# Optimization experiments

Measured on AMD Instinct MI355X. Metric: run time of the kernel, lower is better.

## Reference

```python
import jax, jax.numpy as jnp
import numpy as np

EMBED_DIM = 1024
N_HEADS = 16
HEAD_DIM = EMBED_DIM // N_HEADS
B, T = 1, 4096

def setup_inputs() -> dict:
    key = jax.random.key(0)
    k1, k2, k3 = jax.random.split(key, 3)
    x = jax.random.normal(k1, (B, T, EMBED_DIM), dtype=jnp.float32)
    # match nn.Linear init scale roughly (not required for correctness testing)
    w_qkv = jax.random.normal(k2, (EMBED_DIM, 3 * EMBED_DIM), dtype=jnp.float32) * (EMBED_DIM ** -0.5)
    w_out = jax.random.normal(k3, (EMBED_DIM, EMBED_DIM), dtype=jnp.float32) * (EMBED_DIM ** -0.5)
    return {"x": x, "w_qkv": w_qkv, "w_out": w_out}

def reference(x, w_qkv, w_out):
    b, t, c = x.shape
    qkv = x @ w_qkv                                  # [B,T,3C]
    q, k, v = jnp.split(qkv, 3, axis=-1)
    # [B,T,C] -> [B,H,T,D]
    def heads(a):
        return a.reshape(b, t, N_HEADS, HEAD_DIM).transpose(0, 2, 1, 3)
    q, k, v = heads(q), heads(k), heads(v)
    scale = 1.0 / jnp.sqrt(jnp.asarray(HEAD_DIM, dtype=x.dtype))
    att = jnp.einsum('bhqd,bhkd->bhqk', q, k) * scale  # [B,H,T,T] (full matrix, as in source)
    att = jax.nn.softmax(att, axis=-1)
    y = jnp.einsum('bhqk,bhkd->bhqd', att, v)          # [B,H,T,D]
    y = y.transpose(0, 2, 1, 3).reshape(b, t, c)
    return y @ w_out
```

## Files before the change

kernel.cpp:

```cpp
#include <hip/hip_runtime.h>
#include <hip/hip_bf16.h>

#define T_SEQ 4096
#define C_DIM 1024
#define NH    16
#define HD    64
#define C3    3072

typedef __attribute__((ext_vector_type(8))) short short8;
typedef __attribute__((ext_vector_type(4))) short short4v;
typedef __attribute__((ext_vector_type(4))) float f32x4;
typedef __attribute__((ext_vector_type(16))) float f32x16;

__device__ __forceinline__ short f2bf(float f) {
  union { float f; unsigned u; } v; v.f = f;
  unsigned r = v.u + 0x7FFFu + ((v.u >> 16) & 1u);
  return (short)(r >> 16);
}

__device__ __forceinline__ unsigned cvt_pk_bf16(float lo, float hi) {
  unsigned r;
  asm volatile("v_cvt_pk_bf16_f32 %0, %1, %2" : "=v"(r) : "v"(lo), "v"(hi));
  return r;
}

__device__ __forceinline__ float exp2_fast(float x) {
  return __builtin_amdgcn_exp2f(x);
}

__device__ __forceinline__ float max_half64(float v) {
  return fmaxf(v, __shfl_xor(v, 32, 64));
}

__device__ __forceinline__ float m3(float a, float b, float c) {
  return fmaxf(fmaxf(a, b), c);
}

__device__ __forceinline__ void gld_lds16(const void* g, void* l) {
  __builtin_amdgcn_global_load_lds(
      (const __attribute__((address_space(1))) unsigned int*)g,
      (__attribute__((address_space(3))) unsigned int*)l, 16, 0, 0);
}

__global__ __launch_bounds__(256) void conv_bf16_kernel(const float* __restrict__ in,
                                                        short* __restrict__ out) {
  const size_t i = ((size_t)blockIdx.x * 256 + threadIdx.x) * 8;
  float4 v0 = *(const float4*)(in + i);
  float4 v1 = *(const float4*)(in + i + 4);
  short8 o;
  o[0] = f2bf(v0.x); o[1] = f2bf(v0.y); o[2] = f2bf(v0.z); o[3] = f2bf(v0.w);
  o[4] = f2bf(v1.x); o[5] = f2bf(v1.y); o[6] = f2bf(v1.z); o[7] = f2bf(v1.w);
  *(short8*)(out + i) = o;
}

__global__ void trans_conv_kernel(const float* __restrict__ in, short* __restrict__ out,
                                  int K, int N) {
  __shared__ float t[32][33];
  const int n0 = blockIdx.x * 32, k0 = blockIdx.y * 32;
  const int tx = threadIdx.x, ty = threadIdx.y;
  for (int i = ty; i < 32; i += 8) t[i][tx] = in[(size_t)(k0 + i) * N + n0 + tx];
  __syncthreads();
  for (int i = ty; i < 32; i += 8) out[(size_t)(n0 + i) * K + k0 + tx] = f2bf(t[tx][i]);
}

__device__ __forceinline__ void store_out(short* C, size_t idx, float v) { C[idx] = f2bf(v); }
__device__ __forceinline__ void store_out(float* C, size_t idx, float v) { C[idx] = v; }

template <typename OutT>
__global__ __launch_bounds__(256) void gemm_bt_kernel(const short* __restrict__ A,
                                                      const short* __restrict__ BT,
                                                      OutT* __restrict__ C,
                                                      int M, int N, int K) {
  __shared__ __align__(16) short As[128 * 32];
  __shared__ __align__(16) short Bs[128 * 32];
  const int tid = threadIdx.x;
  const int wid = tid >> 6;
  const int lane = tid & 63;
  const int l15 = lane & 15;
  const int l4 = lane >> 4;
  const int wr = wid >> 1;
  const int wc = wid & 1;
  const int bm = blockIdx.y * 128;
  const int bn = blockIdx.x * 128;

  f32x4 acc[4][4];
#pragma unroll
  for (int m = 0; m < 4; ++m)
#pragma unroll
    for (int n = 0; n < 4; ++n) acc[m][n] = (f32x4){0.f, 0.f, 0.f, 0.f};

  const int ebase = wid * 1024;
  const int e0 = ebase + lane * 8;
  const int r0 = e0 >> 5, c0 = e0 & 31;
  const int r1 = r0 + 16;

  for (int k0 = 0; k0 < K; k0 += 32) {
    __syncthreads();
    gld_lds16(A + (size_t)(bm + r0) * K + k0 + c0, As + ebase);
    gld_lds16(A + (size_t)(bm + r1) * K + k0 + c0, As + ebase + 512);
    gld_lds16(BT + (size_t)(bn + r0) * K + k0 + c0, Bs + ebase);
    gld_lds16(BT + (size_t)(bn + r1) * K + k0 + c0, Bs + ebase + 512);
    __syncthreads();

    short8 a[4], b[4];
#pragma unroll
    for (int m = 0; m < 4; ++m)
      a[m] = *(const short8*)&As[(wr * 64 + m * 16 + l15) * 32 + l4 * 8];
#pragma unroll
    for (int n = 0; n < 4; ++n)
      b[n] = *(const short8*)&Bs[(wc * 64 + n * 16 + l15) * 32 + l4 * 8];
#pragma unroll
    for (int m = 0; m < 4; ++m)
#pragma unroll
      for (int n = 0; n < 4; ++n)
        acc[m][n] = __builtin_amdgcn_mfma_f32_16x16x32_bf16(a[m], b[n], acc[m][n], 0, 0, 0);
  }

#pragma unroll
  for (int m = 0; m < 4; ++m) {
    const int row0 = bm + wr * 64 + m * 16 + l4 * 4;
#pragma unroll
    for (int n = 0; n < 4; ++n) {
      const int col = bn + wc * 64 + n * 16 + l15;
#pragma unroll
      for (int r = 0; r < 4; ++r)
        store_out(C, (size_t)(row0 + r) * N + col, acc[m][n][r]);
    }
  }
}

__global__ __launch_bounds__(256) void repack_v_kernel(const short* __restrict__ qkv,
                                                       short* __restrict__ vT) {
  const int h = blockIdx.x >> 6;
  const int t0 = (blockIdx.x & 63) << 6;
  __shared__ __align__(16) short tile[64][72];
  const int t = threadIdx.x;
  const int r = t >> 3, c = (t & 7) << 3;
#pragma unroll
  for (int i = 0; i < 2; ++i) {
    const int rr = r + i * 32;
    *(short8*)&tile[rr][c] =
        *(const short8*)&qkv[(size_t)(t0 + rr) * C3 + 2048 + h * 64 + c];
  }
  __syncthreads();
  const int d = t >> 3, tt = (t & 7) << 3;
#pragma unroll
  for (int i = 0; i < 2; ++i) {
    const int dd = d + i * 32;
    short8 v;
#pragma unroll
    for (int j = 0; j < 8; ++j) v[j] = tile[tt + j][dd];
    *(short8*)&vT[(size_t)(h * 64 + dd) * T_SEQ + t0 + tt] = v;
  }
}

__global__ __launch_bounds__(512, 4) void attn_kernel(const short* __restrict__ qkv,
                                                      const short* __restrict__ vT,
                                                      short* __restrict__ y) {
  const int bid = blockIdx.x;
  const int xcd = bid & 7, slot = bid >> 3;
  const int h = xcd * 2 + (slot >> 5);
  const int q0 = (slot & 31) * 128;

  const int tid = threadIdx.x;
  const int w = tid >> 6, lane = tid & 63, l31 = lane & 31, l1 = lane >> 5;
  const int g = w >> 2, wg = w & 3;
  const int kvbase = g * (T_SEQ / 2);

  __shared__ __align__(16) short Ks[2][2][4096];
  __shared__ __align__(16) short Vs[2][2][4096];

  short8 qf[4];
  {
    const short* qp = qkv + (size_t)(q0 + wg * 32 + l31) * C3 + h * 64 + l1 * 8;
#pragma unroll
    for (int ks = 0; ks < 4; ++ks) qf[ks] = *(const short8*)(qp + ks * 16);
  }

  short8 ones_frag;
  {
    const short ob = (l31 == 0 || l31 == 4) ? (short)0x3F80 : (short)0;
#pragma unroll
    for (int j = 0; j < 8; ++j) ones_frag[j] = ob;
  }

  f32x16 oa0, oa1, oext;
#pragma unroll
  for (int r = 0; r < 16; ++r) { oa0[r] = 0.f; oa1[r] = 0.f; oext[r] = 0.f; }
  float m_r = -INFINITY;
  const float SCL = 0.125f * 1.44269504f;
  const float TH = 8.0f / SCL;

  const int lr0 = wg * 8 + (lane >> 3);
  const int csw = ((lane & 7) << 3) ^ ((lane >> 3) << 3);
  const short* kpt = qkv + 1024 + h * 64 + csw + (size_t)(kvbase + lr0) * C3;
  const short* vpt = vT + (size_t)(h * 64 + lr0) * T_SEQ + csw + kvbase;
  const int rswz = (l31 & 7) << 3;

  auto stage = [&](int buf) {
#pragma unroll
    for (int i = 0; i < 2; ++i) {
      gld_lds16(kpt + (size_t)i * 32 * C3, &Ks[g][buf][i * 2048 + wg * 512]);
      gld_lds16(vpt + (size_t)i * 32 * T_SEQ, &Vs[g][buf][i * 2048 + wg * 512]);
    }
  };

  stage(0);
  kpt += (size_t)64 * C3;
  vpt += 64;

  const int NT = T_SEQ / 2 / 64;
  for (int t = 0; t < NT; ++t) {
    const int cur = t & 1;
    __builtin_amdgcn_s_barrier();
    if (t + 1 < NT) {
      stage(cur ^ 1);
      kpt += (size_t)64 * C3;
      vpt += 64;
      asm volatile("s_waitcnt vmcnt(4)" ::: "memory");
    } else {
      asm volatile("s_waitcnt vmcnt(0)" ::: "memory");
    }
    __builtin_amdgcn_s_barrier();

    const short* Kb = &Ks[g][cur][0];
    const short* Vb = &Vs[g][cur][0];

    f32x16 s0, s1;
#pragma unroll
    for (int r = 0; r < 16; ++r) { s0[r] = 0.f; s1[r] = 0.f; }
    __builtin_amdgcn_s_setprio(1);
#pragma unroll
    for (int ks = 0; ks < 4; ++ks) {
      const int c = (ks * 16 + l1 * 8) ^ rswz;
      short8 k0 = *(const short8*)&Kb[l31 * 64 + c];
      short8 k1 = *(const short8*)&Kb[(32 + l31) * 64 + c];
      s0 = __builtin_amdgcn_mfma_f32_32x32x16_bf16(k0, qf[ks], s0, 0, 0, 0);
      s1 = __builtin_amdgcn_mfma_f32_32x32x16_bf16(k1, qf[ks], s1, 0, 0, 0);
    }
    __builtin_amdgcn_s_setprio(0);

    float tm;
    {
      float v0 = m3(s0[0], s0[1], s0[2]);
      float v1 = m3(s0[3], s0[4], s0[5]);
      float v2 = m3(s0[6], s0[7], s0[8]);
      float v3 = m3(s0[9], s0[10], s0[11]);
      float v4 = m3(s0[12], s0[13], s0[14]);
      float v5 = fmaxf(s0[15], s1[0]);
      float v6 = m3(s1[1], s1[2], s1[3]);
      float v7 = m3(s1[4], s1[5], s1[6]);
      float v8 = m3(s1[7], s1[8], s1[9]);
      float v9 = m3(s1[10], s1[11], s1[12]);
      float v10 = m3(s1[13], s1[14], s1[15]);
      float w0 = m3(v0, v1, v2);
      float w1 = m3(v3, v4, v5);
      float w2 = m3(v6, v7, v8);
      float w3 = fmaxf(v9, v10);
      tm = fmaxf(m3(w0, w1, w2), w3);
    }

    if (__any(tm > m_r + TH)) {
      const float tmx = max_half64(tm);
      const float mn = fmaxf(m_r, tmx);
      const float al = exp2_fast((m_r - mn) * SCL);
      m_r = mn;
#pragma unroll
      for (int r = 0; r < 16; ++r) { oa0[r] *= al; oa1[r] *= al; }
      oext[0] *= al;
    }
    const float msc = m_r * SCL;
#pragma unroll
    for (int r = 0; r < 16; ++r) s0[r] = exp2_fast(fmaf(s0[r], SCL, -msc));
#pragma unroll
    for (int r = 0; r < 16; ++r) s1[r] = exp2_fast(fmaf(s1[r], SCL, -msc));

    unsigned pw[4][4];
#pragma unroll
    for (int half = 0; half < 2; ++half) {
      const f32x16& sv = half ? s1 : s0;
#pragma unroll
      for (int kk = 0; kk < 2; ++kk) {
        const int ks = half * 2 + kk;
        unsigned x0 = cvt_pk_bf16(sv[kk * 8 + 0], sv[kk * 8 + 1]);
        unsigned y0 = cvt_pk_bf16(sv[kk * 8 + 4], sv[kk * 8 + 5]);
        asm volatile("s_nop 0\n\tv_permlane32_swap_b32 %0, %1" : "+v"(x0), "+v"(y0));
        unsigned x1 = cvt_pk_bf16(sv[kk * 8 + 2], sv[kk * 8 + 3]);
        unsigned y1 = cvt_pk_bf16(sv[kk * 8 + 6], sv[kk * 8 + 7]);
        asm volatile("s_nop 0\n\tv_permlane32_swap_b32 %0, %1" : "+v"(x1), "+v"(y1));
        pw[ks][0] = x0; pw[ks][1] = x1; pw[ks][2] = y0; pw[ks][3] = y1;
      }
    }

    __builtin_amdgcn_s_setprio(1);
#pragma unroll
    for (int ks = 0; ks < 4; ++ks) {
      union { unsigned u[4]; short8 s8; } uu;
      uu.u[0] = pw[ks][0]; uu.u[1] = pw[ks][1]; uu.u[2] = pw[ks][2]; uu.u[3] = pw[ks][3];
      const int c = (ks * 16 + l1 * 8) ^ rswz;
      short8 v0 = *(const short8*)&Vb[l31 * 64 + c];
      short8 v1 = *(const short8*)&Vb[(32 + l31) * 64 + c];
      oa0 = __builtin_amdgcn_mfma_f32_32x32x16_bf16(v0, uu.s8, oa0, 0, 0, 0);
      oa1 = __builtin_amdgcn_mfma_f32_32x32x16_bf16(v1, uu.s8, oa1, 0, 0, 0);
      oext = __builtin_amdgcn_mfma_f32_32x32x16_bf16(ones_frag, uu.s8, oext, 0, 0, 0);
    }
    __builtin_amdgcn_s_setprio(0);
  }

  const float l_r = oext[0];

  __syncthreads();
  float* Oex = (float*)&Vs[0][0][0];
  float* mex = (float*)&Ks[0][0][0];
  const int xslot = wg * 64 + lane;
  if (g == 1) {
#pragma unroll
    for (int r = 0; r < 16; ++r) {
      Oex[r * 256 + xslot] = oa0[r];
      Oex[(16 + r) * 256 + xslot] = oa1[r];
    }
    mex[xslot] = m_r;
    mex[256 + xslot] = l_r;
  }
  __syncthreads();
  if (g == 0) {
    const float m_b = mex[xslot], l_b = mex[256 + xslot];
    const float mm = fmaxf(m_r, m_b);
    const float a = exp2_fast((m_r - mm) * SCL);
    const float b = exp2_fast((m_b - mm) * SCL);
    const float rl = 1.0f / (l_r * a + l_b * b);
    const float ra = a * rl, rb = b * rl;
    const size_t yb = (size_t)(q0 + wg * 32 + l31) * C_DIM + h * 64;
#pragma unroll
    for (int g4 = 0; g4 < 4; ++g4) {
      short4v o0, o1;
#pragma unroll
      for (int j = 0; j < 4; ++j) {
        o0[j] = f2bf(oa0[g4 * 4 + j] * ra + Oex[(g4 * 4 + j) * 256 + xslot] * rb);
        o1[j] = f2bf(oa1[g4 * 4 + j] * ra + Oex[(16 + g4 * 4 + j) * 256 + xslot] * rb);
      }
      *(short4v*)&y[yb + g4 * 8 + l1 * 4] = o0;
      *(short4v*)&y[yb + 32 + g4 * 8 + l1 * 4] = o1;
    }
  }
}

extern "C" void kernel_launch(void* const* d_in, const int* in_sizes, int n_in,
                              void* d_out, int out_size, void* d_ws, size_t ws_size,
                              hipStream_t stream) {
  const float* x = (const float*)d_in[0];
  const float* w_qkv = (const float*)d_in[1];
  const float* w_out = (const float*)d_in[2];
  float* out = (float*)d_out;

  char* ws = (char*)d_ws;
  short* xb = (short*)ws;            ws += (size_t)T_SEQ * C_DIM * 2;
  short* wqT = (short*)ws;           ws += (size_t)C3 * C_DIM * 2;
  short* woT = (short*)ws;           ws += (size_t)C_DIM * C_DIM * 2;
  short* qkv = (short*)ws;           ws += (size_t)T_SEQ * C3 * 2;
  short* vT = (short*)ws;            ws += (size_t)NH * T_SEQ * HD * 2;
  short* y = (short*)ws;             ws += (size_t)T_SEQ * C_DIM * 2;

  conv_bf16_kernel<<<(T_SEQ * C_DIM) / (256 * 8), 256, 0, stream>>>(x, xb);
  trans_conv_kernel<<<dim3(C3 / 32, C_DIM / 32), dim3(32, 8), 0, stream>>>(w_qkv, wqT, C_DIM, C3);
  trans_conv_kernel<<<dim3(C_DIM / 32, C_DIM / 32), dim3(32, 8), 0, stream>>>(w_out, woT, C_DIM, C_DIM);

  gemm_bt_kernel<short><<<dim3(C3 / 128, T_SEQ / 128), 256, 0, stream>>>(xb, wqT, qkv,
                                                                         T_SEQ, C3, C_DIM);
  repack_v_kernel<<<NH * (T_SEQ / 64), 256, 0, stream>>>(qkv, vT);

  attn_kernel<<<512, 512, 0, stream>>>(qkv, vT, y);

  gemm_bt_kernel<float><<<dim3(C_DIM / 128, T_SEQ / 128), 256, 0, stream>>>(y, woT, out,
                                                                            T_SEQ, C_DIM, C_DIM);
}
```

Measured before the change: 183.4 us.

## Restructure attention so each wave handles 64 queries, reusing K/V fragments

The attention kernel moves to 256-thread blocks. Each wave now processes two 32-query sub-tiles (A and B) against 32-key tiles, so each K and V fragment read from LDS feeds two MFMAs. The row sum is now computed with VALU adds plus a cross-lane shuffle instead of an extra ones-matrix MFMA, and the V staging layout and swizzle change to match. This cuts LDS traffic and MFMA work per query, at the cost of more registers per wave and fewer waves per block to hide latency.

```diff
diff --git a/kernel.cpp b/kernel.cpp
--- a/kernel.cpp
+++ b/kernel.cpp
@@ -154,7 +154,7 @@
   }
 }
 
-__global__ __launch_bounds__(512, 4) void attn_kernel(const short* __restrict__ qkv,
+__global__ __launch_bounds__(256, 2) void attn_kernel(const short* __restrict__ qkv,
                                                       const short* __restrict__ vT,
                                                       short* __restrict__ y) {
   const int bid = blockIdx.x;
@@ -164,183 +164,236 @@
 
   const int tid = threadIdx.x;
   const int w = tid >> 6, lane = tid & 63, l31 = lane & 31, l1 = lane >> 5;
-  const int g = w >> 2, wg = w & 3;
+  const int g = w >> 1, wg = w & 1;
   const int kvbase = g * (T_SEQ / 2);
 
-  __shared__ __align__(16) short Ks[2][2][4096];
-  __shared__ __align__(16) short Vs[2][2][4096];
-
-  short8 qf[4];
+  __shared__ __align__(16) short SM[17408];
+
+  short8 qfA[4], qfB[4];
   {
-    const short* qp = qkv + (size_t)(q0 + wg * 32 + l31) * C3 + h * 64 + l1 * 8;
-#pragma unroll
-    for (int ks = 0; ks < 4; ++ks) qf[ks] = *(const short8*)(qp + ks * 16);
-  }
-
-  short8 ones_frag;
-  {
-    const short ob = (l31 == 0 || l31 == 4) ? (short)0x3F80 : (short)0;
-#pragma unroll
-    for (int j = 0; j < 8; ++j) ones_frag[j] = ob;
-  }
-
-  f32x16 oa0, oa1, oext;
-#pragma unroll
-  for (int r = 0; r < 16; ++r) { oa0[r] = 0.f; oa1[r] = 0.f; oext[r] = 0.f; }
-  float m_r = -INFINITY;
+    const short* qp = qkv + (size_t)(q0 + wg * 64 + l31) * C3 + h * 64 + l1 * 8;
+#pragma unroll
+    for (int ks = 0; ks < 4; ++ks) {
+      qfA[ks] = *(const short8*)(qp + ks * 16);
+      qfB[ks] = *(const short8*)(qp + (size_t)32 * C3 + ks * 16);
+    }
+  }
+
+  f32x16 oaA0, oaA1, oaB0, oaB1;
+#pragma unroll
+  for (int r = 0; r < 16; ++r) { oaA0[r] = 0.f; oaA1[r] = 0.f; oaB0[r] = 0.f; oaB1[r] = 0.f; }
+  float mA = -INFINITY, lA = 0.f, mB = -INFINITY, lB = 0.f;
   const float SCL = 0.125f * 1.44269504f;
   const float TH = 8.0f / SCL;
 
-  const int lr0 = wg * 8 + (lane >> 3);
   const int csw = ((lane & 7) << 3) ^ ((lane >> 3) << 3);
-  const short* kpt = qkv + 1024 + h * 64 + csw + (size_t)(kvbase + lr0) * C3;
-  const short* vpt = vT + (size_t)(h * 64 + lr0) * T_SEQ + csw + kvbase;
+  const short* kpt = qkv + 1024 + h * 64 + csw +
+                     (size_t)(kvbase + wg * 16 + (lane >> 3)) * C3;
+  const int lu = (lane & 7) ^ (lane >> 3);
+  const short* vpt = vT + (size_t)(h * 64 + wg * 16 + (lane >> 3) + (lu >> 2) * 32) * T_SEQ +
+                     kvbase + (lu & 3) * 8;
   const int rswz = (l31 & 7) << 3;
 
+  short* const Kbase = SM + g * 4096;
+  short* const Vbase = SM + 8192 + g * 4096;
+
   auto stage = [&](int buf) {
 #pragma unroll
     for (int i = 0; i < 2; ++i) {
-      gld_lds16(kpt + (size_t)i * 32 * C3, &Ks[g][buf][i * 2048 + wg * 512]);
-      gld_lds16(vpt + (size_t)i * 32 * T_SEQ, &Vs[g][buf][i * 2048 + wg * 512]);
+      gld_lds16(kpt + (size_t)i * 8 * C3, Kbase + buf * 2048 + wg * 1024 + i * 512);
+      gld_lds16(vpt + (size_t)i * 8 * T_SEQ, Vbase + buf * 2048 + wg * 1024 + i * 512);
     }
   };
 
   stage(0);
-  kpt += (size_t)64 * C3;
-  vpt += 64;
-
-  const int NT = T_SEQ / 2 / 64;
+  kpt += (size_t)32 * C3;
+  vpt += 32;
+
+  const int NT = (T_SEQ / 2) / 32;
   for (int t = 0; t < NT; ++t) {
     const int cur = t & 1;
     __builtin_amdgcn_s_barrier();
     if (t + 1 < NT) {
       stage(cur ^ 1);
-      kpt += (size_t)64 * C3;
-      vpt += 64;
+      kpt += (size_t)32 * C3;
+      vpt += 32;
       asm volatile("s_waitcnt vmcnt(4)" ::: "memory");
     } else {
       asm volatile("s_waitcnt vmcnt(0)" ::: "memory");
     }
     __builtin_amdgcn_s_barrier();
 
-    const short* Kb = &Ks[g][cur][0];
-    const short* Vb = &Vs[g][cur][0];
-
-    f32x16 s0, s1;
-#pragma unroll
-    for (int r = 0; r < 16; ++r) { s0[r] = 0.f; s1[r] = 0.f; }
+    const short* Kb = Kbase + cur * 2048;
+    const short* Vb = Vbase + cur * 2048;
+
+    f32x16 sA, sB;
+#pragma unroll
+    for (int r = 0; r < 16; ++r) { sA[r] = 0.f; sB[r] = 0.f; }
     __builtin_amdgcn_s_setprio(1);
 #pragma unroll
     for (int ks = 0; ks < 4; ++ks) {
       const int c = (ks * 16 + l1 * 8) ^ rswz;
-      short8 k0 = *(const short8*)&Kb[l31 * 64 + c];
-      short8 k1 = *(const short8*)&Kb[(32 + l31) * 64 + c];
-      s0 = __builtin_amdgcn_mfma_f32_32x32x16_bf16(k0, qf[ks], s0, 0, 0, 0);
-      s1 = __builtin_amdgcn_mfma_f32_32x32x16_bf16(k1, qf[ks], s1, 0, 0, 0);
+      short8 kf = *(const short8*)&Kb[l31 * 64 + c];
+      sA = __builtin_amdgcn_mfma_f32_32x32x16_bf16(kf, qfA[ks], sA, 0, 0, 0);
+      sB = __builtin_amdgcn_mfma_f32_32x32x16_bf16(kf, qfB[ks], sB, 0, 0, 0);
     }
     __builtin_amdgcn_s_setprio(0);
 
-    float tm;
+    float tmA, tmB;
     {
-      float v0 = m3(s0[0], s0[1], s0[2]);
-      float v1 = m3(s0[3], s0[4], s0[5]);
-      float v2 = m3(s0[6], s0[7], s0[8]);
-      float v3 = m3(s0[9], s0[10], s0[11]);
-      float v4 = m3(s0[12], s0[13], s0[14]);
-      float v5 = fmaxf(s0[15], s1[0]);
-      float v6 = m3(s1[1], s1[2], s1[3]);
-      float v7 = m3(s1[4], s1[5], s1[6]);
-      float v8 = m3(s1[7], s1[8], s1[9]);
-      float v9 = m3(s1[10], s1[11], s1[12]);
-      float v10 = m3(s1[13], s1[14], s1[15]);
-      float w0 = m3(v0, v1, v2);
-      float w1 = m3(v3, v4, v5);
-      float w2 = m3(v6, v7, v8);
-      float w3 = fmaxf(v9, v10);
-      tm = fmaxf(m3(w0, w1, w2), w3);
-    }
-
-    if (__any(tm > m_r + TH)) {
-      const float tmx = max_half64(tm);
-      const float mn = fmaxf(m_r, tmx);
-      const float al = exp2_fast((m_r - mn) * SCL);
-      m_r = mn;
-#pragma unroll
-      for (int r = 0; r < 16; ++r) { oa0[r] *= al; oa1[r] *= al; }
-      oext[0] *= al;
-    }
-    const float msc = m_r * SCL;
-#pragma unroll
-    for (int r = 0; r < 16; ++r) s0[r] = exp2_fast(fmaf(s0[r], SCL, -msc));
-#pragma unroll
-    for (int r = 0; r < 16; ++r) s1[r] = exp2_fast(fmaf(s1[r], SCL, -msc));
-
-    unsigned pw[4][4];
-#pragma unroll
-    for (int half = 0; half < 2; ++half) {
-      const f32x16& sv = half ? s1 : s0;
-#pragma unroll
-      for (int kk = 0; kk < 2; ++kk) {
-        const int ks = half * 2 + kk;
-        unsigned x0 = cvt_pk_bf16(sv[kk * 8 + 0], sv[kk * 8 + 1]);
-        unsigned y0 = cvt_pk_bf16(sv[kk * 8 + 4], sv[kk * 8 + 5]);
+      float v0 = m3(sA[0], sA[1], sA[2]);
+      float v1 = m3(sA[3], sA[4], sA[5]);
+      float v2 = m3(sA[6], sA[7], sA[8]);
+      float v3 = m3(sA[9], sA[10], sA[11]);
+      float v4 = m3(sA[12], sA[13], sA[14]);
+      tmA = fmaxf(m3(v0, v1, v2), m3(v3, v4, sA[15]));
+      float u0 = m3(sB[0], sB[1], sB[2]);
+      float u1 = m3(sB[3], sB[4], sB[5]);
+      float u2 = m3(sB[6], sB[7], sB[8]);
+      float u3 = m3(sB[9], sB[10], sB[11]);
+      float u4 = m3(sB[12], sB[13], sB[14]);
+      tmB = fmaxf(m3(u0, u1, u2), m3(u3, u4, sB[15]));
+    }
+
+    if (__any(fmaxf(tmA - mA, tmB - mB) > TH)) {
+      const float txA = max_half64(tmA);
+      const float mnA = fmaxf(mA, txA);
+      const float alA = exp2_fast((mA - mnA) * SCL);
+      mA = mnA; lA *= alA;
+      const float txB = max_half64(tmB);
+      const float mnB = fmaxf(mB, txB);
+      const float alB = exp2_fast((mB - mnB) * SCL);
+      mB = mnB; lB *= alB;
+#pragma unroll
+      for (int r = 0; r < 16; ++r) {
+        oaA0[r] *= alA; oaA1[r] *= alA;
+        oaB0[r] *= alB; oaB1[r] *= alB;
+      }
+    }
+    const float mscA = mA * SCL, mscB = mB * SCL;
+#pragma unroll
+    for (int r = 0; r < 16; ++r) sA[r] = exp2_fast(fmaf(sA[r], SCL, -mscA));
+#pragma unroll
+    for (int r = 0; r < 16; ++r) sB[r] = exp2_fast(fmaf(sB[r], SCL, -mscB));
+
+    {
+      float u[8];
+#pragma unroll
+      for (int r = 0; r < 8; ++r) u[r] = sA[r] + sA[r + 8];
+#pragma unroll
+      for (int r = 0; r < 4; ++r) u[r] += u[r + 4];
+      lA += (u[0] + u[2]) + (u[1] + u[3]);
+#pragma unroll
+      for (int r = 0; r < 8; ++r) u[r] = sB[r] + sB[r + 8];
+#pragma unroll
+      for (int r = 0; r < 4; ++r) u[r] += u[r + 4];
+      lB += (u[0] + u[2]) + (u[1] + u[3]);
+    }
+
+    unsigned pwA[2][4], pwB[2][4];
+#pragma unroll
+    for (int kh = 0; kh < 2; ++kh) {
+      {
+        unsigned x0 = cvt_pk_bf16(sA[kh * 8 + 0], sA[kh * 8 + 1]);
+        unsigned y0 = cvt_pk_bf16(sA[kh * 8 + 4], sA[kh * 8 + 5]);
         asm volatile("s_nop 0\n\tv_permlane32_swap_b32 %0, %1" : "+v"(x0), "+v"(y0));
-        unsigned x1 = cvt_pk_bf16(sv[kk * 8 + 2], sv[kk * 8 + 3]);
-        unsigned y1 = cvt_pk_bf16(sv[kk * 8 + 6], sv[kk * 8 + 7]);
+        unsigned x1 = cvt_pk_bf16(sA[kh * 8 + 2], sA[kh * 8 + 3]);
+        unsigned y1 = cvt_pk_bf16(sA[kh * 8 + 6], sA[kh * 8 + 7]);
         asm volatile("s_nop 0\n\tv_permlane32_swap_b32 %0, %1" : "+v"(x1), "+v"(y1));
-        pw[ks][0] = x0; pw[ks][1] = x1; pw[ks][2] = y0; pw[ks][3] = y1;
+        pwA[kh][0] = x0; pwA[kh][1] = x1; pwA[kh][2] = y0; pwA[kh][3] = y1;
+      }
+      {
+        unsigned x0 = cvt_pk_bf16(sB[kh * 8 + 0], sB[kh * 8 + 1]);
+        unsigned y0 = cvt_pk_bf16(sB[kh * 8 + 4], sB[kh * 8 + 5]);
+        asm volatile("s_nop 0\n\tv_permlane32_swap_b32 %0, %1" : "+v"(x0), "+v"(y0));
+        unsigned x1 = cvt_pk_bf16(sB[kh * 8 + 2], sB[kh * 8 + 3]);
+        unsigned y1 = cvt_pk_bf16(sB[kh * 8 + 6], sB[kh * 8 + 7]);
+        asm volatile("s_nop 0\n\tv_permlane32_swap_b32 %0, %1" : "+v"(x1), "+v"(y1));
+        pwB[kh][0] = x0; pwB[kh][1] = x1; pwB[kh][2] = y0; pwB[kh][3] = y1;
       }
     }
 
     __builtin_amdgcn_s_setprio(1);
 #pragma unroll
-    for (int ks = 0; ks < 4; ++ks) {
-      union { unsigned u[4]; short8 s8; } uu;
-      uu.u[0] = pw[ks][0]; uu.u[1] = pw[ks][1]; uu.u[2] = pw[ks][2]; uu.u[3] = pw[ks][3];
-      const int c = (ks * 16 + l1 * 8) ^ rswz;
-      short8 v0 = *(const short8*)&Vb[l31 * 64 + c];
-      short8 v1 = *(const short8*)&Vb[(32 + l31) * 64 + c];
-      oa0 = __builtin_amdgcn_mfma_f32_32x32x16_bf16(v0, uu.s8, oa0, 0, 0, 0);
-      oa1 = __builtin_amdgcn_mfma_f32_32x32x16_bf16(v1, uu.s8, oa1, 0, 0, 0);
-      oext = __builtin_amdgcn_mfma_f32_32x32x16_bf16(ones_frag, uu.s8, oext, 0, 0, 0);
+    for (int kh = 0; kh < 2; ++kh) {
+      union { unsigned u[4]; short8 s8; } ua, ub;
+      ua.u[0] = pwA[kh][0]; ua.u[1] = pwA[kh][1]; ua.u[2] = pwA[kh][2]; ua.u[3] = pwA[kh][3];
+      ub.u[0] = pwB[kh][0]; ub.u[1] = pwB[kh][1]; ub.u[2] = pwB[kh][2]; ub.u[3] = pwB[kh][3];
+      {
+        const int unit = ((0 * 4 + kh * 2 + l1) ^ (l31 & 7));
+        short8 vf = *(const short8*)&Vb[l31 * 64 + unit * 8];
+        oaA0 = __builtin_amdgcn_mfma_f32_32x32x16_bf16(vf, ua.s8, oaA0, 0, 0, 0);
+        oaB0 = __builtin_amdgcn_mfma_f32_32x32x16_bf16(vf, ub.s8, oaB0, 0, 0, 0);
+      }
+      {
+        const int unit = ((1 * 4 + kh * 2 + l1) ^ (l31 & 7));
+        short8 vf = *(const short8*)&Vb[l31 * 64 + unit * 8];
+        oaA1 = __builtin_amdgcn_mfma_f32_32x32x16_bf16(vf, ua.s8, oaA1, 0, 0, 0);
+        oaB1 = __builtin_amdgcn_mfma_f32_32x32x16_bf16(vf, ub.s8, oaB1, 0, 0, 0);
+      }
     }
     __builtin_amdgcn_s_setprio(0);
   }
 
-  const float l_r = oext[0];
+  lA += __shfl_xor(lA, 32, 64);
+  lB += __shfl_xor(lB, 32, 64);
 
   __syncthreads();
-  float* Oex = (float*)&Vs[0][0][0];
-  float* mex = (float*)&Ks[0][0][0];
-  const int xslot = wg * 64 + lane;
+  float* Oex = (float*)SM;
+  float* mex = ((float*)SM) + 8192;
   if (g == 1) {
+    float* ob = Oex + wg * 4096;
 #pragma unroll
     for (int r = 0; r < 16; ++r) {
-      Oex[r * 256 + xslot] = oa0[r];
-      Oex[(16 + r) * 256 + xslot] = oa1[r];
-    }
-    mex[xslot] = m_r;
-    mex[256 + xslot] = l_r;
+      ob[r * 64 + lane] = oaA0[r];
+      ob[(16 + r) * 64 + lane] = oaA1[r];
+      ob[(32 + r) * 64 + lane] = oaB0[r];
+      ob[(48 + r) * 64 + lane] = oaB1[r];
+    }
+    float4 ml = {mA, lA, mB, lB};
+    *(float4*)&mex[wg * 256 + lane * 4] = ml;
   }
   __syncthreads();
   if (g == 0) {
-    const float m_b = mex[xslot], l_b = mex[256 + xslot];
-    const float mm = fmaxf(m_r, m_b);
-    const float a = exp2_fast((m_r - mm) * SCL);
-    const float b = exp2_fast((m_b - mm) * SCL);
-    const float rl = 1.0f / (l_r * a + l_b * b);
-    const float ra = a * rl, rb = b * rl;
-    const size_t yb = (size_t)(q0 + wg * 32 + l31) * C_DIM + h * 64;
-#pragma unroll
-    for (int g4 = 0; g4 < 4; ++g4) {
-      short4v o0, o1;
-#pragma unroll
-      for (int j = 0; j < 4; ++j) {
-        o0[j] = f2bf(oa0[g4 * 4 + j] * ra + Oex[(g4 * 4 + j) * 256 + xslot] * rb);
-        o1[j] = f2bf(oa1[g4 * 4 + j] * ra + Oex[(16 + g4 * 4 + j) * 256 + xslot] * rb);
-      }
-      *(short4v*)&y[yb + g4 * 8 + l1 * 4] = o0;
-      *(short4v*)&y[yb + 32 + g4 * 8 + l1 * 4] = o1;
+    const float4 ml = *(const float4*)&mex[wg * 256 + lane * 4];
+    const float* ob = Oex + wg * 4096;
+    {
+      const float mm = fmaxf(mA, ml.x);
+      const float a = exp2_fast((mA - mm) * SCL);
+      const float b = exp2_fast((ml.x - mm) * SCL);
+      const float rl = 1.0f / (lA * a + ml.y * b);
+      const float ra = a * rl, rb = b * rl;
+      const size_t yb = (size_t)(q0 + wg * 64 + l31) * C_DIM + h * 64;
+#pragma unroll
+      for (int g4 = 0; g4 < 4; ++g4) {
+        short4v o0, o1;
+#pragma unroll
+        for (int j = 0; j < 4; ++j) {
+          o0[j] = f2bf(oaA0[g4 * 4 + j] * ra + ob[(g4 * 4 + j) * 64 + lane] * rb);
+          o1[j] = f2bf(oaA1[g4 * 4 + j] * ra + ob[(16 + g4 * 4 + j) * 64 + lane] * rb);
+        }
+        *(short4v*)&y[yb + g4 * 8 + l1 * 4] = o0;
+        *(short4v*)&y[yb + 32 + g4 * 8 + l1 * 4] = o1;
+      }
+    }
+    {
+      const float mm = fmaxf(mB, ml.z);
+      const float a = exp2_fast((mB - mm) * SCL);
+      const float b = exp2_fast((ml.z - mm) * SCL);
+      const float rl = 1.0f / (lB * a + ml.w * b);
+      const float ra = a * rl, rb = b * rl;
+      const size_t yb = (size_t)(q0 + wg * 64 + 32 + l31) * C_DIM + h * 64;
+#pragma unroll
+      for (int g4 = 0; g4 < 4; ++g4) {
+        short4v o0, o1;
+#pragma unroll
+        for (int j = 0; j < 4; ++j) {
+          o0[j] = f2bf(oaB0[g4 * 4 + j] * ra + ob[(32 + g4 * 4 + j) * 64 + lane] * rb);
+          o1[j] = f2bf(oaB1[g4 * 4 + j] * ra + ob[(48 + g4 * 4 + j) * 64 + lane] * rb);
+        }
+        *(short4v*)&y[yb + g4 * 8 + l1 * 4] = o0;
+        *(short4v*)&y[yb + 32 + g4 * 8 + l1 * 4] = o1;
+      }
     }
   }
 }
@@ -369,7 +422,7 @@
                                                                          T_SEQ, C3, C_DIM);
   repack_v_kernel<<<NH * (T_SEQ / 64), 256, 0, stream>>>(qkv, vT);
 
-  attn_kernel<<<512, 512, 0, stream>>>(qkv, vT, y);
+  attn_kernel<<<512, 256, 0, stream>>>(qkv, vT, y);
 
   gemm_bt_kernel<float><<<dim3(C_DIM / 128, T_SEQ / 128), 256, 0, stream>>>(y, woT, out,
                                                                             T_SEQ, C_DIM, C_DIM);
```

After: 178.2 us. -2.8%, faster.
